# Kernel optimization log

Measured on AMD Instinct MI355X. Metric: run time of the kernel, lower is better.

## Reference

```python
import jax, jax.numpy as jnp
import numpy as np

B, V, H = 4, 256, 128
BN_EPS = 1e-5


def setup_inputs() -> dict:
    key = jax.random.key(0)
    ks = jax.random.split(key, 20)
    n = lambda k, shape, s=1.0: jax.random.normal(k, shape, dtype=jnp.float32) * s
    return {
        "h": n(ks[0], (B, V, H)),
        "e": n(ks[1], (B, V, V, H)),
        "x": jax.random.uniform(ks[2], (B, V, 2), dtype=jnp.float32),
        "graph": jax.random.randint(ks[3], (B, V, V), 0, 2, dtype=jnp.int32),
        "Uw": n(ks[4], (H, H), 0.05), "Ub": n(ks[5], (H,), 0.05),
        "Vw": n(ks[6], (H, H), 0.05), "Vb": n(ks[7], (H,), 0.05),
        "Aw": n(ks[8], (H, H), 0.05), "Ab": n(ks[9], (H,), 0.05),
        "Bw": n(ks[10], (H, H), 0.05), "Bb": n(ks[11], (H,), 0.05),
        "Cw": n(ks[12], (H, H), 0.05), "Cb": n(ks[13], (H,), 0.05),
        "dw": n(ks[14], (H, 1), 0.05), "db": n(ks[15], (H,), 0.05),
        "ew": n(ks[16], (1, H), 0.05), "eb": n(ks[17], (1,), 0.05),
        "c": n(ks[18], (1,), 0.1),
        "gamma_h": jnp.ones((H,), jnp.float32), "beta_h": jnp.zeros((H,), jnp.float32),
        "gamma_e": jnp.ones((H,), jnp.float32), "beta_e": jnp.zeros((H,), jnp.float32),
    }


def _batchnorm(z, gamma, beta):
    # BatchNorm1d over flattened leading dims (batch statistics, biased var)
    zf = z.reshape(-1, z.shape[-1])
    mu = zf.mean(0)
    var = zf.var(0)
    return (z - mu) * jax.lax.rsqrt(var + BN_EPS) * gamma + beta


def reference(h, e, x, graph, Uw, Ub, Vw, Vb, Aw, Ab, Bw, Bb, Cw, Cb,
              dw, db, ew, eb, c, gamma_h, beta_h, gamma_e, beta_e):
    lin = lambda z, W, b: jnp.einsum('...i,oi->...o', z, W) + b
    Uh = lin(h, Uw, Ub)                      # B V H
    Vh = lin(h, Vw, Vb)                      # B V H (node-j features)
    Ah = lin(h, Aw, Ab)
    Bh = lin(h, Bw, Bb)
    Ce = lin(e, Cw, Cb)                      # B V V H

    # diff[b,i,j] = x_i - x_j  (== x_to - x_from in the torch code)
    diff = x[:, :, None, :] - x[:, None, :, :]          # B V V 2
    d2 = jnp.sum(diff * diff, axis=-1, keepdims=True)   # B V V 1
    dist = jnp.where(d2 > 0, jnp.sqrt(jnp.where(d2 > 0, d2, 1.0)), 0.0)

    # e_ij = Ah_j + Bh_i + Ce_ij + d(|x_i - x_j|)
    e_new = Ah[:, None, :, :] + Bh[:, :, None, :] + Ce + dist * dw[:, 0] + db
    gates = jax.nn.sigmoid(e_new)                        # B V V H
    pa = jax.nn.sigmoid(jnp.einsum('bijh,oh->bijo', e_new, ew) + eb)  # B V V 1

    x_upd = c * jnp.sum(pa * diff, axis=2)               # B V 2

    # aggregate: zero out where graph == 1 (disconnected), sum over j
    msg = jnp.where(graph[..., None] == 1, 0.0, gates * Vh[:, None, :, :])
    h_new = Uh + jnp.sum(msg, axis=2)                    # B V H

    h_new = jax.nn.relu(_batchnorm(h_new, gamma_h, beta_h))
    e_out = jax.nn.relu(_batchnorm(e_new, gamma_e, beta_e))

    return (h + h_new, e + e_out, x + x_upd)
```

## Files before the change

kernel.cpp:

```cpp
#include <hip/hip_runtime.h>
#include <math.h>

#define BB 4
#define VV 256
#define HH 128
#define NBI (BB*VV)
#define NE  (NBI*VV)
#define BN_EPS 1e-5f

typedef _Float16 half8_ __attribute__((ext_vector_type(8)));
typedef float    floatx4 __attribute__((ext_vector_type(4)));
typedef unsigned uintx4  __attribute__((ext_vector_type(4)));

__device__ __forceinline__ float sigmoidf_(float v) {
    return 1.0f / (1.0f + __expf(-v));
}

__device__ __forceinline__ unsigned pk(float x, float y) {
    auto h = __builtin_amdgcn_cvt_pkrtz(x, y);
    return __builtin_bit_cast(unsigned, h);
}

__device__ __forceinline__ float h2f(unsigned short u) {
    _Float16 h = __builtin_bit_cast(_Float16, u);
    return (float)h;
}

__global__ __launch_bounds__(128)
void k1_lin4(const float* __restrict__ h,
             const float* __restrict__ Uw, const float* __restrict__ Ub,
             const float* __restrict__ Vw, const float* __restrict__ Vb,
             const float* __restrict__ Aw, const float* __restrict__ Ab,
             const float* __restrict__ Bw, const float* __restrict__ Bb,
             const float* __restrict__ Cw,
             float* __restrict__ Uh, float* __restrict__ Vh,
             float* __restrict__ Ah, float* __restrict__ Bh,
             unsigned short* __restrict__ cwp)
{
    __shared__ float sh[HH];
    int bi = blockIdx.x;
    int o  = threadIdx.x;

    if (bi < 128) {
        int idx  = bi*128 + o;
        int j    = idx & 7;
        int slot = idx >> 3;
        int lane = slot & 63;
        int tile = slot >> 6;
        int ht   = tile & 7;
        int ks   = tile >> 3;
        int k    = ks*32 + (lane >> 4)*8 + j;
        int hh   = ht*16 + (lane & 15);
        _Float16 hv = (_Float16)Cw[hh*HH + k];
        cwp[idx] = __builtin_bit_cast(unsigned short, hv);
    }

    sh[o] = h[bi*HH + o];
    __syncthreads();

    float su = Ub[o], sv = Vb[o], sa = Ab[o], sb = Bb[o];
    const float4* sh4 = (const float4*)sh;
    const float4* Uw4 = (const float4*)Uw;
    const float4* Vw4 = (const float4*)Vw;
    const float4* Aw4 = (const float4*)Aw;
    const float4* Bw4 = (const float4*)Bw;
    #pragma unroll 8
    for (int k4 = 0; k4 < 32; ++k4) {
        float4 hv = sh4[k4];
        float4 wu = Uw4[o*32 + k4];
        float4 wv = Vw4[o*32 + k4];
        float4 wa = Aw4[o*32 + k4];
        float4 wb = Bw4[o*32 + k4];
        su += hv.x*wu.x + hv.y*wu.y + hv.z*wu.z + hv.w*wu.w;
        sv += hv.x*wv.x + hv.y*wv.y + hv.z*wv.z + hv.w*wv.w;
        sa += hv.x*wa.x + hv.y*wa.y + hv.z*wa.z + hv.w*wa.w;
        sb += hv.x*wb.x + hv.y*wb.y + hv.z*wb.z + hv.w*wb.w;
    }
    Uh[bi*HH + o] = su;
    Vh[bi*HH + o] = sv;
    Ah[bi*HH + o] = sa;
    Bh[bi*HH + o] = sb;
}

__global__ __launch_bounds__(256, 2)
void k2_main(const float* __restrict__ e,
             const float* __restrict__ x,
             const int*   __restrict__ graph,
             const unsigned short* __restrict__ cwp,
             const float* __restrict__ Cb,
             const float* __restrict__ dw, const float* __restrict__ db,
             const float* __restrict__ ew, const float* __restrict__ ebp,
             const float* __restrict__ Uh, const float* __restrict__ Vh,
             const float* __restrict__ Ah, const float* __restrict__ Bh,
             uintx4* __restrict__ stash,
             float* __restrict__ epart,
             float* __restrict__ hacc,
             float* __restrict__ xupd)
{
    __shared__ unsigned short s_b[16384];
    __shared__ float s_dist[256], s_dx[256], s_dy[256];
    __shared__ int   s_g[256];
    __shared__ float s_red[4*HH];

    int tid  = threadIdx.x;
    int bi   = blockIdx.x;
    int b    = bi >> 8;
    int lane = tid & 63;
    int w    = tid >> 6;
    int hl   = lane & 15;
    int q    = lane >> 4;

    {
        const int4* src = (const int4*)cwp;
        int4* dst = (int4*)s_b;
        #pragma unroll
        for (int it = 0; it < 8; ++it) dst[tid + it*256] = src[tid + it*256];
    }

    float xi0 = x[bi*2 + 0], xi1 = x[bi*2 + 1];
    {
        int j = tid;
        float xj0 = x[(b*VV + j)*2 + 0], xj1 = x[(b*VV + j)*2 + 1];
        float dx = xi0 - xj0, dy = xi1 - xj1;
        float d2 = dx*dx + dy*dy;
        s_dx[j] = dx; s_dy[j] = dy;
        s_dist[j] = (d2 > 0.f) ? sqrtf(d2) : 0.f;
        s_g[j] = graph[(size_t)bi*VV + j];
    }

    float pre[8], dwv[8], ewv[8];
    #pragma unroll
    for (int ht = 0; ht < 8; ++ht) {
        int hh = ht*16 + hl;
        pre[ht] = Bh[bi*HH + hh] + Cb[hh] + db[hh];
        dwv[ht] = dw[hh];
        ewv[ht] = ew[hh];
    }
    float ebv = ebp[0];

    __syncthreads();

    float ssum[8] = {0,0,0,0,0,0,0,0};
    float ssq [8] = {0,0,0,0,0,0,0,0};
    float hsum[8] = {0,0,0,0,0,0,0,0};
    float xa0 = 0.f, xa1 = 0.f;

    float4 L[8];
    {
        const float* eA = e + ((size_t)bi*VV + w*32 + hl)*HH + q*8;
        #pragma unroll
        for (int ks = 0; ks < 4; ++ks) {
            L[2*ks]   = *(const float4*)(eA + ks*32);
            L[2*ks+1] = *(const float4*)(eA + ks*32 + 4);
        }
    }

    #pragma unroll
    for (int ch = 0; ch < 4; ++ch) {
        int chunk = ch >> 1, half = ch & 1;
        int j0 = chunk*128 + w*32 + half*16;

        floatx4 acc[8];
        #pragma unroll
        for (int ht = 0; ht < 8; ++ht) acc[ht] = (floatx4){0.f,0.f,0.f,0.f};

        #pragma unroll
        for (int ks = 0; ks < 4; ++ks) {
            union { half8_ h; unsigned u[4]; } a;
            a.u[0] = pk(L[2*ks].x,   L[2*ks].y);
            a.u[1] = pk(L[2*ks].z,   L[2*ks].w);
            a.u[2] = pk(L[2*ks+1].x, L[2*ks+1].y);
            a.u[3] = pk(L[2*ks+1].z, L[2*ks+1].w);
            #pragma unroll
            for (int ht = 0; ht < 8; ++ht) {
                half8_ bf = *(const half8_*)(s_b + ((size_t)((ks*8 + ht)*64 + lane))*8);
                acc[ht] = __builtin_amdgcn_mfma_f32_16x16x32_f16(a.h, bf, acc[ht], 0, 0, 0);
            }
        }

        int jb = j0 + q*4;

        float Avh[2][8], Vvh[2][8];
        #pragma unroll
        for (int u = 0; u < 2; ++u) {
            const float* ap = Ah + ((size_t)(b*VV) + jb + u)*HH + hl;
            const float* vp = Vh + ((size_t)(b*VV) + jb + u)*HH + hl;
            #pragma unroll
            for (int ht = 0; ht < 8; ++ht) {
                Avh[u][ht] = ap[ht*16];
                Vvh[u][ht] = vp[ht*16];
            }
        }

        if (ch < 3) {
            int chn = ch + 1;
            int j0n = (chn >> 1)*128 + w*32 + (chn & 1)*16;
            const float* eA = e + ((size_t)bi*VV + j0n + hl)*HH + q*8;
            #pragma unroll
            for (int ks = 0; ks < 4; ++ks) {
                L[2*ks]   = *(const float4*)(eA + ks*32);
                L[2*ks+1] = *(const float4*)(eA + ks*32 + 4);
            }
        }

        uintx4 st[4];
        #pragma unroll
        for (int u = 0; u < 4; ++u) {
            int j = jb + u;
            float Av[8], Vv[8];
            if (u < 2) {
                #pragma unroll
                for (int ht = 0; ht < 8; ++ht) { Av[ht] = Avh[u][ht]; Vv[ht] = Vvh[u][ht]; }
            } else {
                const float* ap = Ah + ((size_t)(b*VV) + j)*HH + hl;
                const float* vp = Vh + ((size_t)(b*VV) + j)*HH + hl;
                #pragma unroll
                for (int ht = 0; ht < 8; ++ht) { Av[ht] = ap[ht*16]; Vv[ht] = vp[ht*16]; }
            }

            float dist = s_dist[j], dx = s_dx[j], dy = s_dy[j];
            int g = s_g[j];

            float en[8];
            float padot = 0.f;
            #pragma unroll
            for (int ht = 0; ht < 8; ++ht) {
                float v = acc[ht][u] + Av[ht] + pre[ht] + dist*dwv[ht];
                en[ht] = v;
                ssum[ht] += v;
                ssq[ht]  += v*v;
                padot    += v*ewv[ht];
            }
            if (g != 1) {
                #pragma unroll
                for (int ht = 0; ht < 8; ++ht)
                    hsum[ht] += sigmoidf_(en[ht]) * Vv[ht];
            }

            st[u].x = pk(en[0], en[1]);
            st[u].y = pk(en[2], en[3]);
            st[u].z = pk(en[4], en[5]);
            st[u].w = pk(en[6], en[7]);

            padot += __shfl_xor(padot, 1);
            padot += __shfl_xor(padot, 2);
            padot += __shfl_xor(padot, 4);
            padot += __shfl_xor(padot, 8);
            if (hl == 0) {
                float pa = sigmoidf_(padot + ebv);
                xa0 += pa * dx;
                xa1 += pa * dy;
            }
        }

        #pragma unroll
        for (int u = 0; u < 4; ++u)
            __builtin_nontemporal_store(st[u],
                &stash[((size_t)bi*VV + jb + u)*32 + hl]);
    }

    #pragma unroll
    for (int ht = 0; ht < 8; ++ht) {
        ssum[ht] += __shfl_xor(ssum[ht], 16); ssum[ht] += __shfl_xor(ssum[ht], 32);
        ssq[ht]  += __shfl_xor(ssq[ht],  16); ssq[ht]  += __shfl_xor(ssq[ht],  32);
        hsum[ht] += __shfl_xor(hsum[ht], 16); hsum[ht] += __shfl_xor(hsum[ht], 32);
    }

    __syncthreads();
    if (lane < 16) {
        #pragma unroll
        for (int ht = 0; ht < 8; ++ht) s_red[w*HH + ht*16 + lane] = ssum[ht];
    }
    __syncthreads();
    if (tid < HH)
        epart[(size_t)bi*2*HH + tid] =
            s_red[tid] + s_red[HH + tid] + s_red[2*HH + tid] + s_red[3*HH + tid];
    __syncthreads();
    if (lane < 16) {
        #pragma unroll
        for (int ht = 0; ht < 8; ++ht) s_red[w*HH + ht*16 + lane] = ssq[ht];
    }
    __syncthreads();
    if (tid < HH)
        epart[(size_t)bi*2*HH + HH + tid] =
            s_red[tid] + s_red[HH + tid] + s_red[2*HH + tid] + s_red[3*HH + tid];
    __syncthreads();
    if (lane < 16) {
        #pragma unroll
        for (int ht = 0; ht < 8; ++ht) s_red[w*HH + ht*16 + lane] = hsum[ht];
    }
    __syncthreads();
    if (tid < HH)
        hacc[bi*HH + tid] = Uh[bi*HH + tid] +
            s_red[tid] + s_red[HH + tid] + s_red[2*HH + tid] + s_red[3*HH + tid];
    __syncthreads();
    if (hl == 0) { s_red[w*4 + q] = xa0; s_red[16 + w*4 + q] = xa1; }
    __syncthreads();
    if (tid == 0) {
        float sx = 0.f, sy = 0.f;
        #pragma unroll
        for (int t = 0; t < 16; ++t) { sx += s_red[t]; sy += s_red[16 + t]; }
        xupd[bi*2 + 0] = sx;
        xupd[bi*2 + 1] = sy;
    }
}

__global__ __launch_bounds__(256)
void k3_stats(const float* __restrict__ epart, const float* __restrict__ hacc,
              const float* __restrict__ gamma_e, const float* __restrict__ beta_e,
              const float* __restrict__ gamma_h, const float* __restrict__ beta_h,
              float* __restrict__ coefs)
{
    __shared__ float rs[256], rq[256];
    int c = blockIdx.x, tid = threadIdx.x;
    float s = 0, q = 0;
    if (c < HH) {
        for (int r = tid; r < NBI; r += 256) {
            s += epart[(size_t)r*2*HH + c];
            q += epart[(size_t)r*2*HH + HH + c];
        }
    } else {
        int hh = c - HH;
        for (int r = tid; r < NBI; r += 256) {
            float v = hacc[r*HH + hh];
            s += v; q += v*v;
        }
    }
    rs[tid] = s; rq[tid] = q;
    __syncthreads();
    for (int off = 128; off > 0; off >>= 1) {
        if (tid < off) { rs[tid] += rs[tid+off]; rq[tid] += rq[tid+off]; }
        __syncthreads();
    }
    if (tid == 0) {
        float n = (c < HH) ? (float)NE : (float)NBI;
        float mean = rs[0] / n;
        float var  = rq[0] / n - mean*mean;
        int hh; float g, be;
        if (c < HH) { hh = c;      g = gamma_e[hh]; be = beta_e[hh]; }
        else        { hh = c - HH; g = gamma_h[hh]; be = beta_h[hh]; }
        float scale = g * rsqrtf(var + BN_EPS);
        float shift = be - mean*scale;
        if (c < HH) { coefs[hh]        = scale; coefs[HH + hh]   = shift; }
        else        { coefs[2*HH + hh] = scale; coefs[3*HH + hh] = shift; }
    }
}

__global__ __launch_bounds__(256)
void k4_eout(const float* __restrict__ e, const float* __restrict__ coefs,
             const float* __restrict__ h, const float* __restrict__ x,
             const float* __restrict__ hacc, const float* __restrict__ xupd,
             const float* __restrict__ cp,
             float* __restrict__ out0, float* __restrict__ out2,
             float* __restrict__ out1)
{
    __shared__ unsigned short s_t[64*144];
    int tid = threadIdx.x;
    int gid = blockIdx.x*256 + tid;
    if (gid < NBI*HH) {
        int hh = gid & 127;
        float v = hacc[gid]*coefs[2*HH + hh] + coefs[3*HH + hh];
        out0[gid] = h[gid] + fmaxf(v, 0.f);
        if (gid < NBI*2) out2[gid] = x[gid] + cp[0]*xupd[gid];
    }

    size_t r0 = (size_t)blockIdx.x * 64;
    const uintx4* sp = (const uintx4*)out1;
    #pragma unroll
    for (int it = 0; it < 4; ++it) {
        int rr = it*16 + (tid >> 4);
        int sg = tid & 15;
        uintx4 v = __builtin_nontemporal_load(&sp[(r0 + rr)*32 + sg]);
        *(uintx4*)(s_t + rr*144 + sg*8) = v;
    }
    __syncthreads();

    const float4* e4  = (const float4*)e;
    floatx4* o4       = (floatx4*)out1;
    const float4* sc4 = (const float4*)coefs;
    const float4* sh4 = (const float4*)(coefs + HH);
    #pragma unroll
    for (int k = 0; k < 8; ++k) {
        int f  = k*256 + tid;
        int r  = f >> 5;
        int c4 = f & 31;
        size_t gi = (r0 + r)*32 + c4;
        float4 ev = e4[gi];
        float4 sc = sc4[c4], sh = sh4[c4];
        const unsigned short* row = s_t + r*144;
        int cc = c4*4;
        int pb = (cc & 15)*8 + (cc >> 4);
        float4 en;
        en.x = h2f(row[pb]);
        en.y = h2f(row[pb + 8]);
        en.z = h2f(row[pb + 16]);
        en.w = h2f(row[pb + 24]);
        floatx4 rr;
        rr.x = ev.x + fmaxf(en.x*sc.x + sh.x, 0.f);
        rr.y = ev.y + fmaxf(en.y*sc.y + sh.y, 0.f);
        rr.z = ev.z + fmaxf(en.z*sc.z + sh.z, 0.f);
        rr.w = ev.w + fmaxf(en.w*sc.w + sh.w, 0.f);
        __builtin_nontemporal_store(rr, &o4[gi]);
    }
}

extern "C" void kernel_launch(void* const* d_in, const int* in_sizes, int n_in,
                              void* d_out, int out_size, void* d_ws, size_t ws_size,
                              hipStream_t stream)
{
    (void)in_sizes; (void)n_in; (void)out_size; (void)ws_size;
    const float* h     = (const float*)d_in[0];
    const float* e     = (const float*)d_in[1];
    const float* x     = (const float*)d_in[2];
    const int*   graph = (const int*)d_in[3];
    const float* Uw = (const float*)d_in[4];
    const float* Ub = (const float*)d_in[5];
    const float* Vw = (const float*)d_in[6];
    const float* Vb = (const float*)d_in[7];
    const float* Aw = (const float*)d_in[8];
    const float* Ab = (const float*)d_in[9];
    const float* Bw = (const float*)d_in[10];
    const float* Bbv = (const float*)d_in[11];
    const float* Cw = (const float*)d_in[12];
    const float* Cb = (const float*)d_in[13];
    const float* dw = (const float*)d_in[14];
    const float* db = (const float*)d_in[15];
    const float* ew = (const float*)d_in[16];
    const float* eb = (const float*)d_in[17];
    const float* c  = (const float*)d_in[18];
    const float* gamma_h = (const float*)d_in[19];
    const float* beta_h  = (const float*)d_in[20];
    const float* gamma_e = (const float*)d_in[21];
    const float* beta_e  = (const float*)d_in[22];

    float* out0 = (float*)d_out;
    float* out1 = out0 + NBI*HH;
    float* out2 = out1 + (size_t)NE*HH;

    float* ws    = (float*)d_ws;
    float* Uh    = ws;
    float* Vh    = Uh + NBI*HH;
    float* Ah    = Vh + NBI*HH;
    float* Bh    = Ah + NBI*HH;
    float* hacc  = Bh + NBI*HH;
    float* epart = hacc + NBI*HH;
    float* xupd  = epart + (size_t)NBI*2*HH;
    float* coefs = xupd + NBI*2;
    unsigned short* cwp = (unsigned short*)(coefs + 4*HH);

    k1_lin4<<<NBI, 128, 0, stream>>>(h, Uw, Ub, Vw, Vb, Aw, Ab, Bw, Bbv, Cw,
                                     Uh, Vh, Ah, Bh, cwp);
    k2_main<<<NBI, 256, 0, stream>>>(e, x, graph, cwp, Cb, dw, db, ew, eb,
                                     Uh, Vh, Ah, Bh, (uintx4*)out1,
                                     epart, hacc, xupd);
    k3_stats<<<2*HH, 256, 0, stream>>>(epart, hacc, gamma_e, beta_e,
                                       gamma_h, beta_h, coefs);
    k4_eout<<<NE/64, 256, 0, stream>>>(e, coefs, h, x, hacc, xupd, c,
                                       out0, out2, out1);
}
```

Measured before the change: 386.7 us.

## Interleave Ah/Vh into lane-contiguous layout for vector loads in main kernel

The linear kernel now writes Ah and Vh into a single interleaved buffer. Each MFMA lane's 8 Ah and 8 Vh values for a given node j sit contiguously there, so the main kernel loads them with four 16-byte vector loads instead of sixteen strided scalar loads. All loads for the chunk are issued before the MFMA loop to overlap their latency. Launch bounds are also raised to 3 blocks per SM to push occupancy, which risks register spills given the extra 64 live registers.

```diff
diff --git a/kernel.cpp b/kernel.cpp
--- a/kernel.cpp
+++ b/kernel.cpp
@@ -33,8 +33,8 @@
              const float* __restrict__ Aw, const float* __restrict__ Ab,
              const float* __restrict__ Bw, const float* __restrict__ Bb,
              const float* __restrict__ Cw,
-             float* __restrict__ Uh, float* __restrict__ Vh,
-             float* __restrict__ Ah, float* __restrict__ Bh,
+             float* __restrict__ Uh, float* __restrict__ Bh,
+             float* __restrict__ avp,
              unsigned short* __restrict__ cwp)
 {
     __shared__ float sh[HH];
@@ -77,12 +77,13 @@
         sb += hv.x*wb.x + hv.y*wb.y + hv.z*wb.z + hv.w*wb.w;
     }
     Uh[bi*HH + o] = su;
-    Vh[bi*HH + o] = sv;
-    Ah[bi*HH + o] = sa;
     Bh[bi*HH + o] = sb;
-}
-
-__global__ __launch_bounds__(256, 2)
+    int hl = o & 15, ht = o >> 4;
+    avp[bi*256 + hl*16 + ht]     = sa;
+    avp[bi*256 + hl*16 + 8 + ht] = sv;
+}
+
+__global__ __launch_bounds__(256, 3)
 void k2_main(const float* __restrict__ e,
              const float* __restrict__ x,
              const int*   __restrict__ graph,
@@ -90,8 +91,8 @@
              const float* __restrict__ Cb,
              const float* __restrict__ dw, const float* __restrict__ db,
              const float* __restrict__ ew, const float* __restrict__ ebp,
-             const float* __restrict__ Uh, const float* __restrict__ Vh,
-             const float* __restrict__ Ah, const float* __restrict__ Bh,
+             const float* __restrict__ Uh, const float* __restrict__ Bh,
+             const float* __restrict__ avp,
              uintx4* __restrict__ stash,
              float* __restrict__ epart,
              float* __restrict__ hacc,
@@ -159,6 +160,16 @@
     for (int ch = 0; ch < 4; ++ch) {
         int chunk = ch >> 1, half = ch & 1;
         int j0 = chunk*128 + w*32 + half*16;
+        int jb = j0 + q*4;
+
+        floatx4 AV[4][4];
+        #pragma unroll
+        for (int u = 0; u < 4; ++u) {
+            const floatx4* ab =
+                (const floatx4*)(avp + ((size_t)(b*VV) + jb + u)*256 + hl*16);
+            AV[u][0] = ab[0]; AV[u][1] = ab[1];
+            AV[u][2] = ab[2]; AV[u][3] = ab[3];
+        }
 
         floatx4 acc[8];
         #pragma unroll
@@ -178,20 +189,6 @@
             }
         }
 
-        int jb = j0 + q*4;
-
-        float Avh[2][8], Vvh[2][8];
-        #pragma unroll
-        for (int u = 0; u < 2; ++u) {
-            const float* ap = Ah + ((size_t)(b*VV) + jb + u)*HH + hl;
-            const float* vp = Vh + ((size_t)(b*VV) + jb + u)*HH + hl;
-            #pragma unroll
-            for (int ht = 0; ht < 8; ++ht) {
-                Avh[u][ht] = ap[ht*16];
-                Vvh[u][ht] = vp[ht*16];
-            }
-        }
-
         if (ch < 3) {
             int chn = ch + 1;
             int j0n = (chn >> 1)*128 + w*32 + (chn & 1)*16;
@@ -208,14 +205,12 @@
         for (int u = 0; u < 4; ++u) {
             int j = jb + u;
             float Av[8], Vv[8];
-            if (u < 2) {
-                #pragma unroll
-                for (int ht = 0; ht < 8; ++ht) { Av[ht] = Avh[u][ht]; Vv[ht] = Vvh[u][ht]; }
-            } else {
-                const float* ap = Ah + ((size_t)(b*VV) + j)*HH + hl;
-                const float* vp = Vh + ((size_t)(b*VV) + j)*HH + hl;
-                #pragma unroll
-                for (int ht = 0; ht < 8; ++ht) { Av[ht] = ap[ht*16]; Vv[ht] = vp[ht*16]; }
+            #pragma unroll
+            for (int ht = 0; ht < 4; ++ht) {
+                Av[ht]   = AV[u][0][ht];
+                Av[ht+4] = AV[u][1][ht];
+                Vv[ht]   = AV[u][2][ht];
+                Vv[ht+4] = AV[u][3][ht];
             }
 
             float dist = s_dist[j], dx = s_dx[j], dy = s_dy[j];
@@ -439,19 +434,18 @@
 
     float* ws    = (float*)d_ws;
     float* Uh    = ws;
-    float* Vh    = Uh + NBI*HH;
-    float* Ah    = Vh + NBI*HH;
-    float* Bh    = Ah + NBI*HH;
-    float* hacc  = Bh + NBI*HH;
+    float* Bh    = Uh + NBI*HH;
+    float* avp   = Bh + NBI*HH;
+    float* hacc  = avp + (size_t)NBI*256;
     float* epart = hacc + NBI*HH;
     float* xupd  = epart + (size_t)NBI*2*HH;
     float* coefs = xupd + NBI*2;
     unsigned short* cwp = (unsigned short*)(coefs + 4*HH);
 
     k1_lin4<<<NBI, 128, 0, stream>>>(h, Uw, Ub, Vw, Vb, Aw, Ab, Bw, Bbv, Cw,
-                                     Uh, Vh, Ah, Bh, cwp);
+                                     Uh, Bh, avp, cwp);
     k2_main<<<NBI, 256, 0, stream>>>(e, x, graph, cwp, Cb, dw, db, ew, eb,
-                                     Uh, Vh, Ah, Bh, (uintx4*)out1,
+                                     Uh, Bh, avp, (uintx4*)out1,
                                      epart, hacc, xupd);
     k3_stats<<<2*HH, 256, 0, stream>>>(epart, hacc, gamma_e, beta_e,
                                        gamma_h, beta_h, coefs);
```

New measurement: 474.9 us. +22.8%, slower.
